# Performance work log

Hardware: AMD Instinct MI355X
Metric: run time of the kernel (lower is better)

The kernel has to match this reference:

```python
import jax, jax.numpy as jnp
import numpy as np

C, SHOT, D = 64, 16, 320
LN_EPS = 1e-5


def setup_inputs() -> dict:
    key = jax.random.key(0)
    ks = jax.random.split(key, 20)
    s = 0.05
    inp = {
        "input_x_mean": jax.random.normal(ks[0], (C, D), jnp.float32),
        "input_x": jax.random.normal(ks[1], (C * SHOT, D), jnp.float32),
        # embedding_same / embedding_diff Linear(D, D)
        "W_same": jax.random.normal(ks[2], (D, D), jnp.float32) * s,
        "b_same": jnp.zeros((D,), jnp.float32),
        "W_diff": jax.random.normal(ks[3], (D, D), jnp.float32) * s,
        "b_diff": jnp.zeros((D,), jnp.float32),
        # 1-head MultiHeadAttention(d_model=d_k=d_v=D)
        "Wq": jax.random.normal(ks[4], (D, D), jnp.float32) * s,
        "bq": jnp.zeros((D,), jnp.float32),
        "Wk": jax.random.normal(ks[5], (D, D), jnp.float32) * s,
        "bk": jnp.zeros((D,), jnp.float32),
        "Wv": jax.random.normal(ks[6], (D, D), jnp.float32) * s,
        "bv": jnp.zeros((D,), jnp.float32),
        "Wfc": jax.random.normal(ks[7], (D, D), jnp.float32) * s,
        "bfc": jnp.zeros((D,), jnp.float32),
        "ln_g": jnp.ones((D,), jnp.float32),
        "ln_b": jnp.zeros((D,), jnp.float32),
        # output Linear(D, 1)
        "Wout": jax.random.normal(ks[8], (D, 1), jnp.float32) * s,
        "bout": jnp.zeros((1,), jnp.float32),
    }
    return inp


def _mha(q, k, v, Wq, bq, Wk, bk, Wv, bv, Wfc, bfc, ln_g, ln_b):
    # Standard 1-head attention: proj -> scaled softmax attn -> fc -> residual + LayerNorm
    residual = q
    temp = jnp.sqrt(jnp.asarray(q.shape[-1], q.dtype))
    qp = q @ Wq + bq
    kp = k @ Wk + bk
    vp = v @ Wv + bv
    attn = jax.nn.softmax(jnp.einsum('bld,bmd->blm', qp, kp) / temp, axis=-1)
    out = jnp.einsum('blm,bmd->bld', attn, vp)
    out = out @ Wfc + bfc
    out = out + residual
    mu = out.mean(-1, keepdims=True)
    var = ((out - mu) ** 2).mean(-1, keepdims=True)
    return ln_g * (out - mu) * jax.lax.rsqrt(var + LN_EPS) + ln_b


def reference(input_x_mean, input_x, W_same, b_same, W_diff, b_diff,
              Wq, bq, Wk, bk, Wv, bv, Wfc, bfc, ln_g, ln_b, Wout, bout):
    c, d = input_x_mean.shape
    shot = input_x.shape[0] // c
    x = input_x.reshape(c, shot, d)

    # ---- Difference_Estimator ----
    same_diff = x - input_x_mean[:, None, :]                     # (C, shot, D)
    cls = np.arange(c)
    other = np.stack([np.concatenate([cls[:i], cls[i + 1:]]) for i in range(c)])  # (C, C-1)
    idx = (other[:, :, None] * shot + np.arange(shot)[None, None, :]).reshape(c, (c - 1) * shot)
    diff_diff = input_x_mean[:, None, :] - input_x[idx]          # (C, (C-1)*shot, D)

    # ---- Mean_Aggregator (one odefunc evaluation; state = input_x_mean) ----
    ps = (same_diff @ W_same + b_same) - input_x_mean[:, None, :]
    pd = (diff_diff @ W_diff + b_diff) - input_x_mean[:, None, :]
    ts = _mha(ps, ps, ps, Wq, bq, Wk, bk, Wv, bv, Wfc, bfc, ln_g, ln_b)
    td = _mha(pd, pd, pd, Wq, bq, Wk, bk, Wv, bv, Wfc, bfc, ln_g, ln_b)
    sm_s = jax.nn.softmax(ts @ Wout + bout, axis=1)              # (C, shot, 1)
    sm_d = jax.nn.softmax(td @ Wout + bout, axis=1)              # (C, (C-1)*shot, 1)
    weighted = jnp.concatenate([sm_s * ps, sm_d * pd], axis=1)   # (C, C*shot, D)
    return weighted.mean(axis=1)                                 # (C, D)
```

## Files before the change

### kernel.cpp

```cpp
#include <hip/hip_runtime.h>

#define CC   64
#define SHOT 16
#define DD   320
#define ND   1008
#define MS   (CC * SHOT)
#define MD   (CC * ND)
#define MT   (MD + MS)
#define LN_EPS 1e-5f

typedef __attribute__((ext_vector_type(8)))  short short8;
typedef __attribute__((ext_vector_type(4)))  float floatx4;
typedef __attribute__((ext_vector_type(4)))  int i32x4;

__device__ __forceinline__ unsigned short f2b(float f) {
  union { float f; unsigned int u; } v; v.f = f;
  unsigned int r = v.u + 0x7FFFu + ((v.u >> 16) & 1u);
  return (unsigned short)(r >> 16);
}
__device__ __forceinline__ float b2f(unsigned short b) {
  union { unsigned int u; float f; } v; v.u = ((unsigned int)b) << 16; return v.f;
}
__device__ __forceinline__ unsigned int pk2(float a, float b) {
  return (unsigned int)f2b(a) | ((unsigned int)f2b(b) << 16);
}
__device__ __forceinline__ void gl_lds16(const void* g, void* l) {
  __builtin_amdgcn_global_load_lds(
      (const __attribute__((address_space(1))) unsigned int*)g,
      (__attribute__((address_space(3))) unsigned int*)l, 16, 0, 0);
}
__device__ __forceinline__ floatx4 mfma16(short8 a, short8 b, floatx4 c) {
  return __builtin_amdgcn_mfma_f32_16x16x32_bf16(a, b, c, 0, 0, 0);
}
#define BARRIER_VM()  do { asm volatile("s_waitcnt vmcnt(0) lgkmcnt(0)" ::: "memory"); \
                           __builtin_amdgcn_s_barrier(); \
                           __builtin_amdgcn_sched_barrier(0); } while (0)

__global__ __launch_bounds__(256, 2) void gemm_mfma(
    const unsigned short* __restrict__ A,
    const float* __restrict__ Xg, const float* __restrict__ Xmean,
    const int mode,
    const unsigned short* __restrict__ BtDiff,
    const unsigned short* __restrict__ BtSame,
    const float* __restrict__ biasDiff, const float* __restrict__ biasSame,
    unsigned short* __restrict__ OutB,
    const unsigned short* __restrict__ ResB)
{
  __shared__ __align__(16) unsigned short As[2][128 * 64];
  __shared__ __align__(16) unsigned short Bs[2][64 * 64];
  const int t  = threadIdx.x;
  const int m0 = blockIdx.x * 128;
  const int n0 = blockIdx.y * 64;
  const int wid = t >> 6, lane = t & 63;
  const int wm = wid >> 1, wn = wid & 1;
  const int l15 = lane & 15, lg = lane >> 4;

  const bool isDiff = (m0 < MD);
  const unsigned short* Bt = (mode == 3 && !isDiff) ? BtSame : BtDiff;
  const float* bias = (mode == 3 && !isDiff) ? biasSame : biasDiff;

  const int ra = t >> 1, kh = t & 1;
  const float* aptr = nullptr; const float* mptr = nullptr;
  float sa = 1.f;
  if (mode == 3) {
    const int am = m0 + ra;
    if (isDiff) {
      const int c = am / ND, j = am - c * ND;
      const int oi = j >> 4, s = j & 15;
      const int oc = (oi < c) ? oi : oi + 1;
      aptr = Xg + (size_t)(oc * SHOT + s) * DD;
      mptr = Xmean + (size_t)c * DD;
      sa = -1.f;
    } else {
      const int ls = am - MD;
      aptr = Xg + (size_t)ls * DD;
      mptr = Xmean + (size_t)(ls >> 4) * DD;
      sa = 1.f;
    }
  }

  floatx4 acc[4][2];
  #pragma unroll
  for (int i = 0; i < 4; ++i)
    #pragma unroll
    for (int j = 0; j < 2; ++j) acc[i][j] = (floatx4){0.f, 0.f, 0.f, 0.f};

  auto stage = [&](int ks, int bufi) {
    const int k0 = ks * 64;
    #pragma unroll
    for (int it = 0; it < 2; ++it) {
      const int L = it * 256 + t;
      const int r = L >> 3, cs = L & 7;
      const int cl = cs ^ (r & 7);
      gl_lds16(Bt + (size_t)(n0 + r) * DD + k0 + cl * 8, &Bs[bufi][0] + L * 8);
    }
    if (mode == 0) {
      #pragma unroll
      for (int it = 0; it < 4; ++it) {
        const int L = it * 256 + t;
        const int r = L >> 3, cs = L & 7;
        const int cl = cs ^ (r & 7);
        gl_lds16(A + (size_t)(m0 + r) * DD + k0 + cl * 8, &As[bufi][0] + L * 8);
      }
    } else {
      const int kb2 = k0 + kh * 32;
      #pragma unroll
      for (int i = 0; i < 4; ++i) {
        const float4 x0  = *(const float4*)(aptr + kb2 + i * 8);
        const float4 x1  = *(const float4*)(aptr + kb2 + i * 8 + 4);
        const float4 mv0 = *(const float4*)(mptr + kb2 + i * 8);
        const float4 mv1 = *(const float4*)(mptr + kb2 + i * 8 + 4);
        i32x4 w;
        w[0] = (int)pk2(sa * (x0.x - mv0.x), sa * (x0.y - mv0.y));
        w[1] = (int)pk2(sa * (x0.z - mv0.z), sa * (x0.w - mv0.w));
        w[2] = (int)pk2(sa * (x1.x - mv1.x), sa * (x1.y - mv1.y));
        w[3] = (int)pk2(sa * (x1.z - mv1.z), sa * (x1.w - mv1.w));
        const int c  = kh * 4 + i;
        const int cw = c ^ (ra & 7);
        *(i32x4*)((char*)&As[bufi][0] + ra * 128 + cw * 16) = w;
      }
    }
  };

  auto compute = [&](int bufi) {
    #pragma unroll
    for (int kc = 0; kc < 2; ++kc) {
      short8 af[4], bf[2];
      #pragma unroll
      for (int mt = 0; mt < 4; ++mt) {
        const int row = wm * 64 + mt * 16 + l15;
        const int cs  = (kc * 4 + lg) ^ (row & 7);
        af[mt] = *(const short8*)((const char*)&As[bufi][0] + row * 128 + cs * 16);
      }
      #pragma unroll
      for (int nt = 0; nt < 2; ++nt) {
        const int row = wn * 32 + nt * 16 + l15;
        const int cs  = (kc * 4 + lg) ^ (row & 7);
        bf[nt] = *(const short8*)((const char*)&Bs[bufi][0] + row * 128 + cs * 16);
      }
      #pragma unroll
      for (int mt = 0; mt < 4; ++mt)
        #pragma unroll
        for (int nt = 0; nt < 2; ++nt)
          acc[mt][nt] = mfma16(af[mt], bf[nt], acc[mt][nt]);
    }
  };

  stage(0, 0);
  BARRIER_VM();
  for (int ks = 0; ks < 5; ++ks) {
    if (ks + 1 < 5) stage(ks + 1, (ks + 1) & 1);
    compute(ks & 1);
    BARRIER_VM();
  }

  #pragma unroll
  for (int nt = 0; nt < 2; ++nt) {
    const int n = n0 + wn * 32 + nt * 16 + l15;
    const float bb = bias[n];
    #pragma unroll
    for (int mt = 0; mt < 4; ++mt) {
      #pragma unroll
      for (int r = 0; r < 4; ++r) {
        const int m = m0 + wm * 64 + mt * 16 + lg * 4 + r;
        float v = acc[mt][nt][r] + bb;
        if (mode == 3) {
          const int cm = isDiff ? (m / ND) : ((m - MD) >> 4);
          v -= Xmean[(size_t)cm * DD + n];
        }
        if (ResB) v += b2f(ResB[(size_t)m * DD + n]);
        OutB[(size_t)m * DD + n] = f2b(v);
      }
    }
  }
}

__global__ __launch_bounds__(256, 2) void attn16(
    const unsigned short* __restrict__ Qg, const unsigned short* __restrict__ Pk,
    const unsigned short* __restrict__ Pt, unsigned short* __restrict__ Ob,
    const int qRows,
    const int kPitch,
    const int vtPitch,
    const int nKT, const int validKV, const int bpc, const int qTiles)
{
  __shared__ __align__(16) char smem[40960];
  const int t = threadIdx.x;
  const int wid = t >> 6, lane = t & 63;
  const int l15 = lane & 15, lg = lane >> 4;

  int bx = blockIdx.x;
  const int nwg = gridDim.x;
  if ((nwg & 7) == 0) bx = (bx & 7) * (nwg >> 3) + (bx >> 3);
  const int cls  = bx / bpc;
  const int blkq = bx - cls * bpc;
  const int qt0 = blkq * 4 + wid;
  const bool wValid = qt0 < qTiles;
  const int qt = wValid ? qt0 : qTiles - 1;

  short8 qf[10];
  {
    const unsigned short* qrow = Qg + ((size_t)cls * qRows + qt * 16 + l15) * DD;
    #pragma unroll
    for (int kc = 0; kc < 10; ++kc) qf[kc] = *(const short8*)(qrow + kc * 32 + lg * 8);
  }

  floatx4 o[20];
  #pragma unroll
  for (int i = 0; i < 20; ++i) o[i] = (floatx4){0.f, 0.f, 0.f, 0.f};
  float mrun = -1e30f, lsum = 0.f;
  const float scale = 0.05590169943749474f;

  for (int kt = 0; kt < nKT; ++kt) {
    __syncthreads();
    #pragma unroll
    for (int it = 0; it < 5; ++it) {
      const int L = it * 256 + t;
      const int r = L / 40, c = L - (L / 40) * 40;
      const int cl = (c & ~7) | ((c & 7) ^ (r & 7));
      gl_lds16(Pk + ((size_t)cls * kPitch + kt * 32 + r) * DD + cl * 8, smem + L * 16);
    }
    #pragma unroll
    for (int it = 0; it < 5; ++it) {
      const int L = it * 256 + t;
      const int d = L >> 2, c = L & 3;
      const int cl = c ^ ((d >> 1) & 3);
      gl_lds16(Pt + ((size_t)cls * DD + d) * vtPitch + kt * 32 + cl * 8,
               smem + 20480 + L * 16);
    }
    __syncthreads();

    floatx4 st0 = (floatx4){0.f,0.f,0.f,0.f}, st1 = (floatx4){0.f,0.f,0.f,0.f};
    __builtin_amdgcn_s_setprio(1);
    #pragma unroll
    for (int kc = 0; kc < 10; ++kc) {
      const int c = kc * 4 + lg;
      const int cl = (c & ~7) | ((c & 7) ^ (l15 & 7));
      const short8 k0f = *(const short8*)(smem + l15 * 640 + cl * 16);
      const short8 k1f = *(const short8*)(smem + (16 + l15) * 640 + cl * 16);
      st0 = mfma16(k0f, qf[kc], st0);
      st1 = mfma16(k1f, qf[kc], st1);
    }
    __builtin_amdgcn_s_setprio(0);

    float s[8];
    #pragma unroll
    for (int r = 0; r < 4; ++r) { s[r] = st0[r] * scale; s[4 + r] = st1[r] * scale; }
    const int kvb = kt * 32 + lg * 4;
    #pragma unroll
    for (int r = 0; r < 4; ++r) {
      if (kvb + r      >= validKV) s[r]     = -1e30f;
      if (kvb + 16 + r >= validKV) s[4 + r] = -1e30f;
    }
    float mt_ = s[0];
    #pragma unroll
    for (int i = 1; i < 8; ++i) mt_ = fmaxf(mt_, s[i]);
    mt_ = fmaxf(mt_, __shfl_xor(mt_, 16));
    mt_ = fmaxf(mt_, __shfl_xor(mt_, 32));
    if (!__all(mt_ - mrun <= 8.0f)) {
      const float newm = fmaxf(mrun, mt_);
      const float alpha = __expf(mrun - newm);
      lsum *= alpha;
      #pragma unroll
      for (int i = 0; i < 20; ++i) {
        o[i][0] *= alpha; o[i][1] *= alpha; o[i][2] *= alpha; o[i][3] *= alpha;
      }
      mrun = newm;
    }
    float p[8]; float rs = 0.f;
    #pragma unroll
    for (int i = 0; i < 8; ++i) { p[i] = __expf(s[i] - mrun); rs += p[i]; }
    rs += __shfl_xor(rs, 16);
    rs += __shfl_xor(rs, 32);
    lsum += rs;

    const unsigned int pk00 = pk2(p[0], p[1]), pk01 = pk2(p[2], p[3]);
    const unsigned int pk10 = pk2(p[4], p[5]), pk11 = pk2(p[6], p[7]);
    const int src0 = l15 + ((lane >> 4) & 1) * 32;
    const int src1 = src0 + 16;
    const int y0 = __shfl((int)pk00, src0), y1 = __shfl((int)pk01, src0);
    const int y2 = __shfl((int)pk00, src1), y3 = __shfl((int)pk01, src1);
    const int z0 = __shfl((int)pk10, src0), z1 = __shfl((int)pk11, src0);
    const int z2 = __shfl((int)pk10, src1), z3 = __shfl((int)pk11, src1);
    const bool hi = lane >= 32;
    union { i32x4 w; short8 v; } pf;
    pf.w[0] = hi ? z0 : y0; pf.w[1] = hi ? z1 : y1;
    pf.w[2] = hi ? z2 : y2; pf.w[3] = hi ? z3 : y3;

    const int vswz = (l15 >> 1) & 3;
    __builtin_amdgcn_s_setprio(1);
    #pragma unroll
    for (int dt = 0; dt < 20; ++dt) {
      const int d = dt * 16 + l15;
      const short8 a = *(const short8*)(smem + 20480 + d * 64 + ((lg ^ vswz) << 4));
      o[dt] = mfma16(a, pf.v, o[dt]);
    }
    __builtin_amdgcn_s_setprio(0);
  }

  const float invl = 1.f / lsum;
  __syncthreads();
  char* ep = smem + wid * 10240;
  #pragma unroll
  for (int dt = 0; dt < 20; ++dt) {
    const unsigned int w0 = pk2(o[dt][0] * invl, o[dt][1] * invl);
    const unsigned int w1 = pk2(o[dt][2] * invl, o[dt][3] * invl);
    *(unsigned int*)(ep + l15 * 640 + (dt * 16 + lg * 4) * 2)     = w0;
    *(unsigned int*)(ep + l15 * 640 + (dt * 16 + lg * 4 + 2) * 2) = w1;
  }
  __syncthreads();
  if (wValid) {
    #pragma unroll
    for (int it = 0; it < 10; ++it) {
      const int flat = it * 64 + lane;
      const int q = flat / 40, c = flat - (flat / 40) * 40;
      const i32x4 v = *(const i32x4*)(ep + q * 640 + c * 16);
      *(i32x4*)(Ob + ((size_t)cls * qRows + qt * 16 + q) * DD + c * 8) = v;
    }
  }
}

__global__ __launch_bounds__(256) void transpose_p(
    const unsigned short* __restrict__ P, unsigned short* __restrict__ PtG,
    const int rowsP, const int vtPitch, const int kvTilesPerCls)
{
  __shared__ __align__(16) unsigned short Ls[64 * 72];
  const int t = threadIdx.x;
  const int cls = blockIdx.x / kvTilesPerCls;
  const int kvt = blockIdx.x - cls * kvTilesPerCls;
  const int dt = blockIdx.y;
  #pragma unroll
  for (int i = 0; i < 2; ++i) {
    const int flat = t + i * 256;
    const int r = flat >> 3, c = flat & 7;
    const int kv = kvt * 64 + r;
    i32x4 v = {0, 0, 0, 0};
    if (kv < rowsP)
      v = *(const i32x4*)(P + ((size_t)cls * rowsP + kv) * DD + dt * 64 + c * 8);
    *(i32x4*)(&Ls[r * 72 + c * 8]) = v;
  }
  __syncthreads();
  #pragma unroll
  for (int i = 0; i < 2; ++i) {
    const int flat = t + i * 256;
    const int r2 = flat >> 3, c2 = flat & 7;
    if (kvt * 64 + c2 * 8 < vtPitch) {
      union { unsigned short e[8]; i32x4 v; } u;
      #pragma unroll
      for (int jj = 0; jj < 8; ++jj) u.e[jj] = Ls[(c2 * 8 + jj) * 72 + r2];
      *(i32x4*)(PtG + ((size_t)cls * DD + dt * 64 + r2) * vtPitch + kvt * 64 + c2 * 8) = u.v;
    }
  }
}

__global__ __launch_bounds__(256) void wprep(
    const float* __restrict__ Wsame, const float* __restrict__ Wdiff,
    const float* __restrict__ Wk, const float* __restrict__ Wq,
    const float* __restrict__ Wfc, const float* __restrict__ Wv,
    unsigned short* __restrict__ BtS, unsigned short* __restrict__ BtD,
    unsigned short* __restrict__ BtG, unsigned short* __restrict__ BtVF)
{
  __shared__ float Ls[64 * 68];
  const int t = threadIdx.x;
  const int z = blockIdx.z;
  if (z < 2) {
    const float* W = z ? Wdiff : Wsame;
    unsigned short* Wt = z ? BtD : BtS;
    const int k0 = blockIdx.x * 64, n0 = blockIdx.y * 64;
    #pragma unroll
    for (int i = 0; i < 4; ++i) {
      const int flat = t + i * 256;
      const int r = flat >> 4, c = (flat & 15) * 4;
      *(float4*)&Ls[r * 68 + c] = *(const float4*)(W + (size_t)(k0 + r) * DD + n0 + c);
    }
    __syncthreads();
    #pragma unroll
    for (int j = 0; j < 2; ++j) {
      const int flat = t + j * 256;
      const int r2 = flat >> 3, c2 = flat & 7;
      union { unsigned short e[8]; i32x4 v; } u;
      #pragma unroll
      for (int jj = 0; jj < 8; ++jj) u.e[jj] = f2b(Ls[(c2 * 8 + jj) * 68 + r2]);
      *(i32x4*)(Wt + (size_t)(n0 + r2) * DD + k0 + c2 * 8) = u.v;
    }
  } else {
    const int trL = (z == 3);
    const float* L = trL ? Wfc : Wk;
    const float* R = trL ? Wv : Wq;
    float* Lsm = Ls;
    float* Rsm = Ls + 16 * 68;
    const int n0 = blockIdx.x * 64, k0 = blockIdx.y * 64;
    const int tn4 = (t & 15) * 4, tk4 = (t >> 4) * 4;
    float acc[4][4] = {};
    for (int ms = 0; ms < DD; ms += 16) {
      const int lr = t >> 4, lc = (t & 15);
      #pragma unroll
      for (int i = 0; i < 4; ++i) {
        const int nn = lc * 4 + i;
        Lsm[lr * 68 + nn] = trL ? L[(size_t)(ms + lr) * DD + n0 + nn]
                                : L[(size_t)(n0 + nn) * DD + ms + lr];
        Rsm[lr * 68 + nn] = R[(size_t)(k0 + nn) * DD + ms + lr];
      }
      __syncthreads();
      #pragma unroll
      for (int mm = 0; mm < 16; ++mm) {
        float la[4], rb[4];
        #pragma unroll
        for (int i = 0; i < 4; ++i) { la[i] = Lsm[mm * 68 + tn4 + i]; rb[i] = Rsm[mm * 68 + tk4 + i]; }
        #pragma unroll
        for (int i = 0; i < 4; ++i)
          #pragma unroll
          for (int j = 0; j < 4; ++j) acc[i][j] += la[i] * rb[j];
      }
      __syncthreads();
    }
    #pragma unroll
    for (int i = 0; i < 4; ++i)
      #pragma unroll
      for (int j = 0; j < 4; ++j)
        ((z == 2) ? BtG : BtVF)[(size_t)(n0 + tn4 + i) * DD + k0 + tk4 + j] = f2b(acc[i][j]);
  }
}

__global__ __launch_bounds__(640) void wbias(
    const float* __restrict__ Wk, const float* __restrict__ bq,
    const float* __restrict__ Wfc, const float* __restrict__ bv,
    const float* __restrict__ bfc, float* __restrict__ v, float* __restrict__ bvf)
{
  const int t = threadIdx.x;
  if (t < DD) {
    float a = 0.f;
    for (int m = 0; m < DD; ++m) a += Wk[(size_t)t * DD + m] * bq[m];
    v[t] = a;
  } else if (t < 2 * DD) {
    const int n = t - DD;
    float a = 0.f;
    for (int m = 0; m < DD; ++m) a += Wfc[(size_t)m * DD + n] * bv[m];
    bvf[n] = a + bfc[n];
  }
}

__global__ __launch_bounds__(256) void ln_logit(
    const unsigned short* __restrict__ X, const float* __restrict__ gam,
    const float* __restrict__ bet, const float* __restrict__ Wout,
    const float* __restrict__ bout, float* __restrict__ logits, const int M)
{
  const int row = blockIdx.x * 4 + (threadIdx.x >> 6);
  if (row >= M) return;
  const int lane = threadIdx.x & 63;
  const unsigned short* x = X + (size_t)row * DD;
  float v[5]; float s = 0.f;
  #pragma unroll
  for (int i = 0; i < 5; ++i) { v[i] = b2f(x[lane + 64 * i]); s += v[i]; }
  #pragma unroll
  for (int off = 32; off; off >>= 1) s += __shfl_xor(s, off);
  const float mu = s * (1.f / DD);
  float q = 0.f;
  #pragma unroll
  for (int i = 0; i < 5; ++i) { const float d = v[i] - mu; q += d * d; }
  #pragma unroll
  for (int off = 32; off; off >>= 1) q += __shfl_xor(q, off);
  const float inv = rsqrtf(q * (1.f / DD) + LN_EPS);
  float lg = 0.f;
  #pragma unroll
  for (int i = 0; i < 5; ++i) {
    const int k = lane + 64 * i;
    lg += (gam[k] * (v[i] - mu) * inv + bet[k]) * Wout[k];
  }
  #pragma unroll
  for (int off = 32; off; off >>= 1) lg += __shfl_xor(lg, off);
  if (lane == 0) logits[row] = lg + bout[0];
}

__global__ __launch_bounds__(320) void final_reduce(
    const float* __restrict__ logits_s, const float* __restrict__ logits_d,
    const unsigned short* __restrict__ Ps, const unsigned short* __restrict__ Pd,
    float* __restrict__ out)
{
  const int c = blockIdx.x;
  const int t = threadIdx.x;
  __shared__ float w[16 + ND];
  __shared__ float red[5];
  if (t < 16) w[t] = logits_s[c * 16 + t];
  for (int j = t; j < ND; j += 320) w[16 + j] = logits_d[c * ND + j];
  __syncthreads();
  if (t == 0) {
    float mx = w[0];
    #pragma unroll
    for (int i = 1; i < 16; ++i) mx = fmaxf(mx, w[i]);
    float ssum = 0.f;
    #pragma unroll
    for (int i = 0; i < 16; ++i) { const float e = __expf(w[i] - mx); w[i] = e; ssum += e; }
    const float inv = 1.f / ssum;
    #pragma unroll
    for (int i = 0; i < 16; ++i) w[i] *= inv;
  }
  float lm = -1e30f;
  for (int j = t; j < ND; j += 320) lm = fmaxf(lm, w[16 + j]);
  #pragma unroll
  for (int off = 32; off; off >>= 1) lm = fmaxf(lm, __shfl_xor(lm, off));
  if ((t & 63) == 0) red[t >> 6] = lm;
  __syncthreads();
  const float mx = fmaxf(fmaxf(fmaxf(red[0], red[1]), fmaxf(red[2], red[3])), red[4]);
  float ls = 0.f;
  for (int j = t; j < ND; j += 320) { const float e = __expf(w[16 + j] - mx); w[16 + j] = e; ls += e; }
  #pragma unroll
  for (int off = 32; off; off >>= 1) ls += __shfl_xor(ls, off);
  __syncthreads();
  if ((t & 63) == 0) red[t >> 6] = ls;
  __syncthreads();
  const float inv = 1.f / (red[0] + red[1] + red[2] + red[3] + red[4]);
  for (int j = t; j < ND; j += 320) w[16 + j] *= inv;
  __syncthreads();
  float acc = 0.f;
  const unsigned short* Psc = Ps + (size_t)c * SHOT * DD + t;
  const unsigned short* Pdc = Pd + (size_t)c * ND * DD + t;
  #pragma unroll 4
  for (int i = 0; i < 16; ++i) acc += w[i] * b2f(Psc[(size_t)i * DD]);
  for (int j = 0; j < ND; ++j) acc += w[16 + j] * b2f(Pdc[(size_t)j * DD]);
  out[c * DD + t] = acc * (1.f / 1024.f);
}

extern "C" void kernel_launch(void* const* d_in, const int* in_sizes, int n_in,
                              void* d_out, int out_size, void* d_ws, size_t ws_size,
                              hipStream_t stream)
{
  const float* xmean = (const float*)d_in[0];
  const float* x     = (const float*)d_in[1];
  const float* Wsame = (const float*)d_in[2];
  const float* bsame = (const float*)d_in[3];
  const float* Wdiff = (const float*)d_in[4];
  const float* bdiff = (const float*)d_in[5];
  const float* Wq    = (const float*)d_in[6];
  const float* bq    = (const float*)d_in[7];
  const float* Wk    = (const float*)d_in[8];
  const float* bk    = (const float*)d_in[9];   (void)bk;
  const float* Wv    = (const float*)d_in[10];
  const float* bv    = (const float*)d_in[11];
  const float* Wfc   = (const float*)d_in[12];
  const float* bfc   = (const float*)d_in[13];
  const float* lng   = (const float*)d_in[14];
  const float* lnb   = (const float*)d_in[15];
  const float* Wout  = (const float*)d_in[16];
  const float* boutp = (const float*)d_in[17];
  float* outp = (float*)d_out;

  char* base = (char*)d_ws;
  size_t off = 0;
  auto alloc = [&](size_t bytes) { char* p = base + off; off += (bytes + 255) & ~(size_t)255; return p; };

  const size_t WB = (size_t)DD * DD * 2;
  unsigned short* BtS  = (unsigned short*)alloc(WB);
  unsigned short* BtD  = (unsigned short*)alloc(WB);
  unsigned short* BtG  = (unsigned short*)alloc(WB);
  unsigned short* BtVF = (unsigned short*)alloc(WB);
  float* vbias = (float*)alloc(DD * 4);
  float* bvf   = (float*)alloc(DD * 4);
  unsigned short* P_b  = (unsigned short*)alloc((size_t)MT * DD * 2);
  unsigned short* Qg_b = (unsigned short*)alloc((size_t)MT * DD * 2);
  unsigned short* O_b  = (unsigned short*)alloc((size_t)MT * DD * 2);
  unsigned short* PtD  = (unsigned short*)alloc((size_t)CC * DD * 1024 * 2);
  unsigned short* PtS  = (unsigned short*)alloc((size_t)CC * DD * 32 * 2);
  float* logits = (float*)alloc((size_t)MT * 4);

  const dim3 blk(256);
  wprep<<<dim3(5, 5, 4), blk, 0, stream>>>(Wsame, Wdiff, Wk, Wq, Wfc, Wv,
                                           BtS, BtD, BtG, BtVF);
  wbias<<<dim3(1), dim3(640), 0, stream>>>(Wk, bq, Wfc, bv, bfc, vbias, bvf);

  const dim3 gAll(MT / 128, 5);
  gemm_mfma<<<gAll, blk, 0, stream>>>(nullptr, x, xmean, 3, BtD, BtS,
                                      bdiff, bsame, P_b, nullptr);
  transpose_p<<<dim3(CC * 16, 5), blk, 0, stream>>>(P_b, PtD, ND, 1024, 16);
  transpose_p<<<dim3(CC, 5), blk, 0, stream>>>(P_b + (size_t)MD * DD, PtS, 16, 32, 1);
  gemm_mfma<<<gAll, blk, 0, stream>>>(P_b, nullptr, nullptr, 0, BtG, nullptr,
                                      vbias, nullptr, Qg_b, nullptr);
  attn16<<<dim3(CC * 16), blk, 0, stream>>>(Qg_b, P_b, PtD, O_b,
                                            ND, ND, 1024, 32, ND, 16, 63);
  attn16<<<dim3(CC), blk, 0, stream>>>(Qg_b + (size_t)MD * DD, P_b + (size_t)MD * DD,
                                       PtS, O_b + (size_t)MD * DD,
                                       16, 16, 32, 1, 16, 1, 1);
  gemm_mfma<<<gAll, blk, 0, stream>>>(O_b, nullptr, nullptr, 0, BtVF, nullptr,
                                      bvf, nullptr, Qg_b, P_b);
  ln_logit<<<dim3(MT / 4), blk, 0, stream>>>(Qg_b, lng, lnb, Wout, boutp, logits, MT);
  final_reduce<<<dim3(CC), dim3(320), 0, stream>>>(logits + MD, logits,
                                                   P_b + (size_t)MD * DD, P_b, outp);
}
```

Before: 492.0 us.

## Merge attention launches, fold bias prep into wprep, split final reduce, swizzle LDS

Both attention calls (diff and same sets) now run as one launch that picks its parameters from the block index, and the wbias kernel is folded into wprep as an extra z slice, which removes two launches. The final reduction gets five times as many blocks, each handling 64 columns with the 1008-row sum split across five thread groups and combined in shared memory. The attention epilogue now XOR-swizzles its LDS staging to cut bank conflicts. In exchange the attention kernel carries branchy per-block setup, and the final reduce recomputes the softmax normalisation in every column block.

```diff
diff --git a/kernel.cpp b/kernel.cpp
--- a/kernel.cpp
+++ b/kernel.cpp
@@ -176,12 +176,9 @@
 }
 
 __global__ __launch_bounds__(256, 2) void attn16(
-    const unsigned short* __restrict__ Qg, const unsigned short* __restrict__ Pk,
-    const unsigned short* __restrict__ Pt, unsigned short* __restrict__ Ob,
-    const int qRows,
-    const int kPitch,
-    const int vtPitch,
-    const int nKT, const int validKV, const int bpc, const int qTiles)
+    const unsigned short* __restrict__ Qall, const unsigned short* __restrict__ Pall,
+    const unsigned short* __restrict__ PtD, const unsigned short* __restrict__ PtS,
+    unsigned short* __restrict__ Oall)
 {
   __shared__ __align__(16) char smem[40960];
   const int t = threadIdx.x;
@@ -189,10 +186,19 @@
   const int l15 = lane & 15, lg = lane >> 4;
 
   int bx = blockIdx.x;
-  const int nwg = gridDim.x;
-  if ((nwg & 7) == 0) bx = (bx & 7) * (nwg >> 3) + (bx >> 3);
-  const int cls  = bx / bpc;
-  const int blkq = bx - cls * bpc;
+  const unsigned short *Qg, *Pk, *Pt; unsigned short* Ob;
+  int cls, blkq, qRows, kPitch, vtPitch, nKT, validKV, qTiles;
+  if (bx < 1024) {
+    bx = (bx & 7) * 128 + (bx >> 3);
+    cls = bx >> 4; blkq = bx & 15;
+    Qg = Qall; Pk = Pall; Pt = PtD; Ob = Oall;
+    qRows = ND; kPitch = ND; vtPitch = 1024; nKT = 32; validKV = ND; qTiles = 63;
+  } else {
+    cls = bx - 1024; blkq = 0;
+    Qg = Qall + (size_t)MD * DD; Pk = Pall + (size_t)MD * DD;
+    Pt = PtS; Ob = Oall + (size_t)MD * DD;
+    qRows = 16; kPitch = 16; vtPitch = 32; nKT = 1; validKV = 16; qTiles = 1;
+  }
   const int qt0 = blkq * 4 + wid;
   const bool wValid = qt0 < qTiles;
   const int qt = wValid ? qt0 : qTiles - 1;
@@ -300,12 +306,13 @@
   const float invl = 1.f / lsum;
   __syncthreads();
   char* ep = smem + wid * 10240;
+  const int qx = (l15 & 7) << 4;
   #pragma unroll
   for (int dt = 0; dt < 20; ++dt) {
     const unsigned int w0 = pk2(o[dt][0] * invl, o[dt][1] * invl);
     const unsigned int w1 = pk2(o[dt][2] * invl, o[dt][3] * invl);
-    *(unsigned int*)(ep + l15 * 640 + (dt * 16 + lg * 4) * 2)     = w0;
-    *(unsigned int*)(ep + l15 * 640 + (dt * 16 + lg * 4 + 2) * 2) = w1;
+    *(unsigned int*)(ep + l15 * 640 + (((dt * 16 + lg * 4) * 2) ^ qx))     = w0;
+    *(unsigned int*)(ep + l15 * 640 + (((dt * 16 + lg * 4 + 2) * 2) ^ qx)) = w1;
   }
   __syncthreads();
   if (wValid) {
@@ -313,7 +320,7 @@
     for (int it = 0; it < 10; ++it) {
       const int flat = it * 64 + lane;
       const int q = flat / 40, c = flat - (flat / 40) * 40;
-      const i32x4 v = *(const i32x4*)(ep + q * 640 + c * 16);
+      const i32x4 v = *(const i32x4*)(ep + q * 640 + ((c * 16) ^ ((q & 7) << 4)));
       *(i32x4*)(Ob + ((size_t)cls * qRows + qt * 16 + q) * DD + c * 8) = v;
     }
   }
@@ -356,8 +363,11 @@
     const float* __restrict__ Wsame, const float* __restrict__ Wdiff,
     const float* __restrict__ Wk, const float* __restrict__ Wq,
     const float* __restrict__ Wfc, const float* __restrict__ Wv,
+    const float* __restrict__ bq, const float* __restrict__ bv,
+    const float* __restrict__ bfc,
     unsigned short* __restrict__ BtS, unsigned short* __restrict__ BtD,
-    unsigned short* __restrict__ BtG, unsigned short* __restrict__ BtVF)
+    unsigned short* __restrict__ BtG, unsigned short* __restrict__ BtVF,
+    float* __restrict__ vbias, float* __restrict__ bvf)
 {
   __shared__ float Ls[64 * 68];
   const int t = threadIdx.x;
@@ -382,7 +392,7 @@
       for (int jj = 0; jj < 8; ++jj) u.e[jj] = f2b(Ls[(c2 * 8 + jj) * 68 + r2]);
       *(i32x4*)(Wt + (size_t)(n0 + r2) * DD + k0 + c2 * 8) = u.v;
     }
-  } else {
+  } else if (z < 4) {
     const int trL = (z == 3);
     const float* L = trL ? Wfc : Wk;
     const float* R = trL ? Wv : Wq;
@@ -418,24 +428,21 @@
       #pragma unroll
       for (int j = 0; j < 4; ++j)
         ((z == 2) ? BtG : BtVF)[(size_t)(n0 + tn4 + i) * DD + k0 + tk4 + j] = f2b(acc[i][j]);
-  }
-}
-
-__global__ __launch_bounds__(640) void wbias(
-    const float* __restrict__ Wk, const float* __restrict__ bq,
-    const float* __restrict__ Wfc, const float* __restrict__ bv,
-    const float* __restrict__ bfc, float* __restrict__ v, float* __restrict__ bvf)
-{
-  const int t = threadIdx.x;
-  if (t < DD) {
-    float a = 0.f;
-    for (int m = 0; m < DD; ++m) a += Wk[(size_t)t * DD + m] * bq[m];
-    v[t] = a;
-  } else if (t < 2 * DD) {
-    const int n = t - DD;
-    float a = 0.f;
-    for (int m = 0; m < DD; ++m) a += Wfc[(size_t)m * DD + n] * bv[m];
-    bvf[n] = a + bfc[n];
+  } else {
+    if (blockIdx.x == 0) {
+      const int n0 = blockIdx.y * 64;
+      if (t < 64) {
+        const int n = n0 + t;
+        float a = 0.f;
+        for (int m = 0; m < DD; ++m) a += Wk[(size_t)n * DD + m] * bq[m];
+        vbias[n] = a;
+      } else if (t < 128) {
+        const int n = n0 + t - 64;
+        float a = 0.f;
+        for (int m = 0; m < DD; ++m) a += Wfc[(size_t)m * DD + n] * bv[m];
+        bvf[n] = a + bfc[n];
+      }
+    }
   }
 }
 
@@ -477,9 +484,11 @@
     float* __restrict__ out)
 {
   const int c = blockIdx.x;
+  const int dt = blockIdx.y;
   const int t = threadIdx.x;
   __shared__ float w[16 + ND];
   __shared__ float red[5];
+  __shared__ float accs[5][64];
   if (t < 16) w[t] = logits_s[c * 16 + t];
   for (int j = t; j < ND; j += 320) w[16 + j] = logits_d[c * ND + j];
   __syncthreads();
@@ -511,13 +520,21 @@
   const float inv = 1.f / (red[0] + red[1] + red[2] + red[3] + red[4]);
   for (int j = t; j < ND; j += 320) w[16 + j] *= inv;
   __syncthreads();
+  const int col = dt * 64 + (t & 63);
+  const int jg  = t >> 6;
   float acc = 0.f;
-  const unsigned short* Psc = Ps + (size_t)c * SHOT * DD + t;
-  const unsigned short* Pdc = Pd + (size_t)c * ND * DD + t;
-  #pragma unroll 4
-  for (int i = 0; i < 16; ++i) acc += w[i] * b2f(Psc[(size_t)i * DD]);
-  for (int j = 0; j < ND; ++j) acc += w[16 + j] * b2f(Pdc[(size_t)j * DD]);
-  out[c * DD + t] = acc * (1.f / 1024.f);
+  const unsigned short* Psc = Ps + (size_t)c * SHOT * DD + col;
+  const unsigned short* Pdc = Pd + (size_t)c * ND * DD + col;
+  if (jg == 0) {
+    #pragma unroll
+    for (int i = 0; i < 16; ++i) acc += w[i] * b2f(Psc[(size_t)i * DD]);
+  }
+  for (int j = jg; j < ND; j += 5) acc += w[16 + j] * b2f(Pdc[(size_t)j * DD]);
+  accs[jg][t & 63] = acc;
+  __syncthreads();
+  if (t < 64)
+    out[c * DD + dt * 64 + t] =
+        (accs[0][t] + accs[1][t] + accs[2][t] + accs[3][t] + accs[4][t]) * (1.f / 1024.f);
 }
 
 extern "C" void kernel_launch(void* const* d_in, const int* in_sizes, int n_in,
@@ -563,9 +580,9 @@
   float* logits = (float*)alloc((size_t)MT * 4);
 
   const dim3 blk(256);
-  wprep<<<dim3(5, 5, 4), blk, 0, stream>>>(Wsame, Wdiff, Wk, Wq, Wfc, Wv,
-                                           BtS, BtD, BtG, BtVF);
-  wbias<<<dim3(1), dim3(640), 0, stream>>>(Wk, bq, Wfc, bv, bfc, vbias, bvf);
+  wprep<<<dim3(5, 5, 5), blk, 0, stream>>>(Wsame, Wdiff, Wk, Wq, Wfc, Wv,
+                                           bq, bv, bfc,
+                                           BtS, BtD, BtG, BtVF, vbias, bvf);
 
   const dim3 gAll(MT / 128, 5);
   gemm_mfma<<<gAll, blk, 0, stream>>>(nullptr, x, xmean, 3, BtD, BtS,
@@ -574,14 +591,10 @@
   transpose_p<<<dim3(CC, 5), blk, 0, stream>>>(P_b + (size_t)MD * DD, PtS, 16, 32, 1);
   gemm_mfma<<<gAll, blk, 0, stream>>>(P_b, nullptr, nullptr, 0, BtG, nullptr,
                                       vbias, nullptr, Qg_b, nullptr);
-  attn16<<<dim3(CC * 16), blk, 0, stream>>>(Qg_b, P_b, PtD, O_b,
-                                            ND, ND, 1024, 32, ND, 16, 63);
-  attn16<<<dim3(CC), blk, 0, stream>>>(Qg_b + (size_t)MD * DD, P_b + (size_t)MD * DD,
-                                       PtS, O_b + (size_t)MD * DD,
-                                       16, 16, 32, 1, 16, 1, 1);
+  attn16<<<dim3(1088), blk, 0, stream>>>(Qg_b, P_b, PtD, PtS, O_b);
   gemm_mfma<<<gAll, blk, 0, stream>>>(O_b, nullptr, nullptr, 0, BtVF, nullptr,
                                       bvf, nullptr, Qg_b, P_b);
   ln_logit<<<dim3(MT / 4), blk, 0, stream>>>(Qg_b, lng, lnb, Wout, boutp, logits, MT);
-  final_reduce<<<dim3(CC), dim3(320), 0, stream>>>(logits + MD, logits,
-                                                   P_b + (size_t)MD * DD, P_b, outp);
-}
+  final_reduce<<<dim3(CC, 5), dim3(320), 0, stream>>>(logits + MD, logits,
+                                                      P_b + (size_t)MD * DD, P_b, outp);
+}
```

New measurement: 478.1 us. -2.8%, faster.
